# Performance work log

Hardware: AMD Instinct MI355X
Metric: run time of the kernel (lower is better)

The kernel has to match this reference:

```python
import jax, jax.numpy as jnp
import numpy as np

BIG = 1e30  # finite stand-in for +inf to keep grads clean


def _chamfer_loss(bin_center, ground_truth):
    # bin_center: [B, n_bins, 1] 1-D 'point cloud' of bin centers
    # ground_truth: [B, 1, H, W] depth map
    B = bin_center.shape[0]
    c = bin_center[..., 0]                      # [B, nb]
    p = ground_truth.reshape(B, -1)             # [B, V] flattened depth points
    mask = p >= 0.001                           # valid (non-near-zero) depths
    n = jnp.sum(mask, axis=1)                   # [B] valid count per sample
    Lmax = jnp.max(n)                           # pad_sequence pads every sample to L_max
    npad = (Lmax - n).astype(c.dtype)           # number of zero pad-points per sample

    # pairwise squared distances between bin centers and depth points
    D = (c[:, :, None] - p[:, None, :]) ** 2    # [B, nb, V]

    # direction 1: gt points -> nearest bin center (sum over points)
    dmin_p = jnp.min(D, axis=1)                 # [B, V]
    sumA = jnp.sum(jnp.where(mask, dmin_p, 0.0), axis=1)
    # each zero pad-point contributes min_j c_j^2
    c2 = c ** 2                                 # [B, nb]
    sumA = sumA + npad * jnp.min(c2, axis=1)

    # direction 2: bin centers -> nearest gt point (incl. zero pad-points if any)
    Dm = jnp.where(mask[:, None, :], D, jnp.asarray(BIG, D.dtype))
    min_valid = jnp.min(Dm, axis=2)             # [B, nb] min over valid points
    has_pad = (npad > 0)[:, None]
    min_b = jnp.where(has_pad, jnp.minimum(min_valid, c2), min_valid)
    sumB = jnp.sum(min_b, axis=1)               # [B]

    # chamferdist: point_reduction=sum, batch_reduction=mean, bidirectional
    return jnp.mean(sumA + sumB)


def setup_inputs() -> dict:
    key = jax.random.key(0)
    k1, k2 = jax.random.split(key)
    bin_center = jax.random.uniform(k1, (4, 256, 1), dtype=jnp.float32)
    ground_truth = jax.random.uniform(k2, (4, 1, 352, 448), dtype=jnp.float32)
    return {"bin_center": bin_center, "ground_truth": ground_truth}


def reference(bin_center, ground_truth):
    return _chamfer_loss(bin_center, ground_truth)
```

## Files before the change

kernel.cpp:

```cpp
#include <hip/hip_runtime.h>

#define NB   256
#define TPB  256
#define NI   (NB + 1)
#define G    128
#define MINF 1e30f
#define CAPD 1e15f

__global__ __launch_bounds__(NB) void k_sort(const float* __restrict__ bc,
                                             float* __restrict__ sbins,
                                             unsigned* __restrict__ gmin,
                                             unsigned* __restrict__ gmax) {
    __shared__ float s[NB];
    const int tid = threadIdx.x, b = blockIdx.x;
    s[tid] = bc[b * NB + tid];
    for (int t = tid; t < NI; t += NB) {
        gmin[b * NI + t] = 0xFFFFFFFFu;
        gmax[b * NI + t] = 0u;
    }
    __syncthreads();
    for (int k = 2; k <= NB; k <<= 1)
        for (int j = k >> 1; j > 0; j >>= 1) {
            const int ixj = tid ^ j;
            if (ixj > tid) {
                const float a = s[tid], bv = s[ixj];
                if ((a > bv) == ((tid & k) == 0)) { s[tid] = bv; s[ixj] = a; }
            }
            __syncthreads();
        }
    sbins[b * NB + tid] = s[tid];
}

__global__ __launch_bounds__(TPB) void k_main(
    const float* __restrict__ sbins, const float* __restrict__ gt,
    int V, int CH,
    float* __restrict__ sumA_part, int* __restrict__ cnt_part,
    unsigned* __restrict__ gmin, unsigned* __restrict__ gmax)
{
    const int b   = blockIdx.x / G;
    const int blk = blockIdx.x % G;
    const int tid = threadIdx.x;
    const int start = blk * CH;
    const int cn = min(CH, V - start);
    const float* __restrict__ gp = gt + (size_t)b * V + start;

    __shared__ float    c[NB];
    __shared__ unsigned imn[NI], imx[NI];
    c[tid] = sbins[b * NB + tid];
    for (int t = tid; t < NI; t += TPB) { imn[t] = 0xFFFFFFFFu; imx[t] = 0u; }
    __syncthreads();

    float sum = 0.f; int cnt = 0;
    for (int i = tid; i < cn; i += TPB) {
        const float q = gp[i];
        if (q >= 0.001f) {
            int idx = 0;
            #pragma unroll
            for (int st = 128; st >= 1; st >>= 1)
                idx += (c[idx + st - 1] <= q) ? st : 0;
            idx += (c[idx] <= q) ? 1 : 0;
            const float dlo = (idx > 0)  ? (q - c[idx - 1]) : MINF;
            const float dhi = (idx < NB) ? (c[idx] - q)     : MINF;
            const float d = fminf(dlo, dhi);
            sum += d * d; ++cnt;
            atomicMin(&imn[idx], __float_as_uint(q));
            atomicMax(&imx[idx], __float_as_uint(q));
        }
    }
    __syncthreads();

    for (int t = tid; t < NI; t += TPB) {
        const unsigned lo = imn[t], hi = imx[t];
        if (lo != 0xFFFFFFFFu) atomicMin(&gmin[b * NI + t], lo);
        if (hi != 0u)          atomicMax(&gmax[b * NI + t], hi);
    }

    for (int off = 32; off; off >>= 1) {
        sum += __shfl_down(sum, off);
        cnt += __shfl_down(cnt, off);
    }
    __shared__ float r4[4]; __shared__ int i4[4];
    if ((tid & 63) == 0) { r4[tid >> 6] = sum; i4[tid >> 6] = cnt; }
    __syncthreads();
    if (tid == 0) {
        sumA_part[blockIdx.x] = r4[0] + r4[1] + r4[2] + r4[3];
        cnt_part [blockIdx.x] = i4[0] + i4[1] + i4[2] + i4[3];
    }
}

__global__ __launch_bounds__(TPB) void k_final(
    const float* __restrict__ sbins,
    const float* __restrict__ sumA_part, const int* __restrict__ cnt_part,
    const unsigned* __restrict__ gmin, const unsigned* __restrict__ gmax,
    int B, float* __restrict__ out)
{
    const int tid = threadIdx.x;
    __shared__ float pm[NB], sm[NB];
    __shared__ float r4[4]; __shared__ int i4[4]; __shared__ float q4[4];
    __shared__ float ssa[8]; __shared__ int sn[8];

    for (int bb = 0; bb < B; ++bb) {
        float s = 0.f; int cc = 0;
        for (int k = tid; k < G; k += TPB) {
            s  += sumA_part[bb * G + k];
            cc += cnt_part [bb * G + k];
        }
        for (int off = 32; off; off >>= 1) { s += __shfl_down(s, off); cc += __shfl_down(cc, off); }
        if ((tid & 63) == 0) { r4[tid >> 6] = s; i4[tid >> 6] = cc; }
        __syncthreads();
        if (tid == 0) { ssa[bb] = r4[0]+r4[1]+r4[2]+r4[3]; sn[bb] = i4[0]+i4[1]+i4[2]+i4[3]; }
        __syncthreads();
    }
    int Lmax = 0;
    for (int bb = 0; bb < B; ++bb) Lmax = max(Lmax, sn[bb]);

    float total = 0.f;
    for (int bb = 0; bb < B; ++bb) {
        const unsigned hib = gmax[bb * NI + tid];
        const unsigned lob = gmin[bb * NI + tid + 1];
        pm[tid] = (hib == 0u)          ? -MINF : __uint_as_float(hib);
        sm[tid] = (lob == 0xFFFFFFFFu) ?  MINF : __uint_as_float(lob);
        __syncthreads();
        for (int off = 1; off < NB; off <<= 1) {
            const float vp = pm[tid], vs = sm[tid];
            const float op = (tid >= off)     ? pm[tid - off] : -MINF;
            const float os = (tid + off < NB) ? sm[tid + off] :  MINF;
            __syncthreads();
            pm[tid] = fmaxf(vp, op);
            sm[tid] = fminf(vs, os);
            __syncthreads();
        }
        const float cj = sbins[bb * NB + tid];
        const float c2 = cj * cj;
        const float d  = fminf(fminf(cj - pm[tid], sm[tid] - cj), CAPD);
        float bm = d * d;
        const int npad = Lmax - sn[bb];
        if (npad > 0) bm = fminf(bm, c2);
        float s = bm, mc = c2;
        for (int off = 32; off; off >>= 1) {
            s  += __shfl_down(s, off);
            mc  = fminf(mc, __shfl_down(mc, off));
        }
        if ((tid & 63) == 0) { r4[tid >> 6] = s; q4[tid >> 6] = mc; }
        __syncthreads();
        if (tid == 0)
            total += ssa[bb]
                   + (float)npad * fminf(fminf(q4[0], q4[1]), fminf(q4[2], q4[3]))
                   + (r4[0] + r4[1] + r4[2] + r4[3]);
        __syncthreads();
    }
    if (tid == 0) out[0] = total / (float)B;
}

extern "C" void kernel_launch(void* const* d_in, const int* in_sizes, int n_in,
                              void* d_out, int out_size, void* d_ws, size_t ws_size,
                              hipStream_t stream) {
    const float* bc = (const float*)d_in[0];
    const float* gt = (const float*)d_in[1];
    const int B  = in_sizes[0] / NB;
    const int V  = in_sizes[1] / B;
    const int CH = (V + G - 1) / G;

    float*    sbins     = (float*)d_ws;
    float*    sumA_part = sbins + (size_t)B * NB;
    int*      cnt_part  = (int*)(sumA_part + (size_t)B * G);
    unsigned* gmin      = (unsigned*)(cnt_part + (size_t)B * G);
    unsigned* gmax      = gmin + (size_t)B * NI;

    k_sort <<<B, NB, 0, stream>>>(bc, sbins, gmin, gmax);
    k_main <<<B * G, TPB, 0, stream>>>(sbins, gt, V, CH,
                                       sumA_part, cnt_part, gmin, gmax);
    k_final<<<1, TPB, 0, stream>>>(sbins, sumA_part, cnt_part,
                                   gmin, gmax, B, (float*)d_out);
}
```

Measured before the change: 78.26 us.

## Fuse sort, main pass and final reduction into one kernel with last-block finish

Replaces the three kernels (bin sort, main pass, single-block final) with one fused kernel. Every block re-sorts the bins in shared memory and computes its own bin-to-point nearest distance from its local min/max tables, merging the result into a global per-bin atomicMin. The last block to finish, found with an atomic counter, performs the final reduction. This removes two kernel launches and the separate scan in the final kernel, at the cost of a redundant bitonic sort and prefix scan in every block plus an extra memset launch.

```diff
diff --git a/kernel.cpp b/kernel.cpp
--- a/kernel.cpp
+++ b/kernel.cpp
@@ -7,49 +7,46 @@
 #define MINF 1e30f
 #define CAPD 1e15f
 
-__global__ __launch_bounds__(NB) void k_sort(const float* __restrict__ bc,
-                                             float* __restrict__ sbins,
-                                             unsigned* __restrict__ gmin,
-                                             unsigned* __restrict__ gmax) {
-    __shared__ float s[NB];
-    const int tid = threadIdx.x, b = blockIdx.x;
-    s[tid] = bc[b * NB + tid];
-    for (int t = tid; t < NI; t += NB) {
-        gmin[b * NI + t] = 0xFFFFFFFFu;
-        gmax[b * NI + t] = 0u;
-    }
+__global__ __launch_bounds__(TPB) void k_fused(
+    const float* __restrict__ bc, const float* __restrict__ gt,
+    int B, int V, int CH,
+    unsigned* __restrict__ gbin,
+    unsigned* __restrict__ counter,
+    unsigned* __restrict__ ssort,
+    unsigned* __restrict__ sumP,
+    unsigned* __restrict__ cntP,
+    float* __restrict__ out)
+{
+    const int b   = blockIdx.x / G;
+    const int blk = blockIdx.x % G;
+    const int tid = threadIdx.x;
+
+    __shared__ float    c[NB];
+    __shared__ unsigned imn[NI], imx[NI];
+    __shared__ float    pm[NB], sm[NB];
+    __shared__ float r4[4]; __shared__ int i4[4]; __shared__ float q4[4];
+    __shared__ float ssa[8]; __shared__ int sn[8];
+    __shared__ unsigned s_old;
+
+    c[tid] = bc[b * NB + tid];
+    for (int t = tid; t < NI; t += TPB) { imn[t] = 0xFFFFFFFFu; imx[t] = 0u; }
     __syncthreads();
+
     for (int k = 2; k <= NB; k <<= 1)
         for (int j = k >> 1; j > 0; j >>= 1) {
             const int ixj = tid ^ j;
             if (ixj > tid) {
-                const float a = s[tid], bv = s[ixj];
-                if ((a > bv) == ((tid & k) == 0)) { s[tid] = bv; s[ixj] = a; }
+                const float a = c[tid], bv = c[ixj];
+                if ((a > bv) == ((tid & k) == 0)) { c[tid] = bv; c[ixj] = a; }
             }
             __syncthreads();
         }
-    sbins[b * NB + tid] = s[tid];
-}
 
-__global__ __launch_bounds__(TPB) void k_main(
-    const float* __restrict__ sbins, const float* __restrict__ gt,
-    int V, int CH,
-    float* __restrict__ sumA_part, int* __restrict__ cnt_part,
-    unsigned* __restrict__ gmin, unsigned* __restrict__ gmax)
-{
-    const int b   = blockIdx.x / G;
-    const int blk = blockIdx.x % G;
-    const int tid = threadIdx.x;
+    if (blk == 0) atomicExch(&ssort[b * NB + tid], __float_as_uint(c[tid]));
+
     const int start = blk * CH;
     const int cn = min(CH, V - start);
     const float* __restrict__ gp = gt + (size_t)b * V + start;
-
-    __shared__ float    c[NB];
-    __shared__ unsigned imn[NI], imx[NI];
-    c[tid] = sbins[b * NB + tid];
-    for (int t = tid; t < NI; t += TPB) { imn[t] = 0xFFFFFFFFu; imx[t] = 0u; }
-    __syncthreads();
-
     float sum = 0.f; int cnt = 0;
     for (int i = tid; i < cn; i += TPB) {
         const float q = gp[i];
@@ -69,41 +66,46 @@
     }
     __syncthreads();
 
-    for (int t = tid; t < NI; t += TPB) {
-        const unsigned lo = imn[t], hi = imx[t];
-        if (lo != 0xFFFFFFFFu) atomicMin(&gmin[b * NI + t], lo);
-        if (hi != 0u)          atomicMax(&gmax[b * NI + t], hi);
+    pm[tid] = (imx[tid]     == 0u)          ? -MINF : __uint_as_float(imx[tid]);
+    sm[tid] = (imn[tid + 1] == 0xFFFFFFFFu) ?  MINF : __uint_as_float(imn[tid + 1]);
+    __syncthreads();
+    for (int off = 1; off < NB; off <<= 1) {
+        const float vp = pm[tid], vs = sm[tid];
+        const float op = (tid >= off)     ? pm[tid - off] : -MINF;
+        const float os = (tid + off < NB) ? sm[tid + off] :  MINF;
+        __syncthreads();
+        pm[tid] = fmaxf(vp, op);
+        sm[tid] = fminf(vs, os);
+        __syncthreads();
+    }
+    {
+        const float cj = c[tid];
+        const float d  = fminf(fminf(cj - pm[tid], sm[tid] - cj), CAPD);
+        atomicMin(&gbin[b * NB + tid], __float_as_uint(d * d));
     }
 
     for (int off = 32; off; off >>= 1) {
         sum += __shfl_down(sum, off);
         cnt += __shfl_down(cnt, off);
     }
-    __shared__ float r4[4]; __shared__ int i4[4];
     if ((tid & 63) == 0) { r4[tid >> 6] = sum; i4[tid >> 6] = cnt; }
     __syncthreads();
     if (tid == 0) {
-        sumA_part[blockIdx.x] = r4[0] + r4[1] + r4[2] + r4[3];
-        cnt_part [blockIdx.x] = i4[0] + i4[1] + i4[2] + i4[3];
+        atomicExch(&sumP[blockIdx.x], __float_as_uint(r4[0] + r4[1] + r4[2] + r4[3]));
+        atomicExch(&cntP[blockIdx.x], (unsigned)(i4[0] + i4[1] + i4[2] + i4[3]));
     }
-}
 
-__global__ __launch_bounds__(TPB) void k_final(
-    const float* __restrict__ sbins,
-    const float* __restrict__ sumA_part, const int* __restrict__ cnt_part,
-    const unsigned* __restrict__ gmin, const unsigned* __restrict__ gmax,
-    int B, float* __restrict__ out)
-{
-    const int tid = threadIdx.x;
-    __shared__ float pm[NB], sm[NB];
-    __shared__ float r4[4]; __shared__ int i4[4]; __shared__ float q4[4];
-    __shared__ float ssa[8]; __shared__ int sn[8];
+    __syncthreads();
+    if (tid == 0) s_old = atomicAdd(counter, 1u);
+    __syncthreads();
+    if (s_old != (unsigned)(gridDim.x - 2)) return;
+    __threadfence();
 
     for (int bb = 0; bb < B; ++bb) {
         float s = 0.f; int cc = 0;
         for (int k = tid; k < G; k += TPB) {
-            s  += sumA_part[bb * G + k];
-            cc += cnt_part [bb * G + k];
+            s  += __uint_as_float(sumP[bb * G + k]);
+            cc += (int)cntP[bb * G + k];
         }
         for (int off = 32; off; off >>= 1) { s += __shfl_down(s, off); cc += __shfl_down(cc, off); }
         if ((tid & 63) == 0) { r4[tid >> 6] = s; i4[tid >> 6] = cc; }
@@ -116,25 +118,10 @@
 
     float total = 0.f;
     for (int bb = 0; bb < B; ++bb) {
-        const unsigned hib = gmax[bb * NI + tid];
-        const unsigned lob = gmin[bb * NI + tid + 1];
-        pm[tid] = (hib == 0u)          ? -MINF : __uint_as_float(hib);
-        sm[tid] = (lob == 0xFFFFFFFFu) ?  MINF : __uint_as_float(lob);
-        __syncthreads();
-        for (int off = 1; off < NB; off <<= 1) {
-            const float vp = pm[tid], vs = sm[tid];
-            const float op = (tid >= off)     ? pm[tid - off] : -MINF;
-            const float os = (tid + off < NB) ? sm[tid + off] :  MINF;
-            __syncthreads();
-            pm[tid] = fmaxf(vp, op);
-            sm[tid] = fminf(vs, os);
-            __syncthreads();
-        }
-        const float cj = sbins[bb * NB + tid];
+        const int   npad = Lmax - sn[bb];
+        const float cj = __uint_as_float(ssort[bb * NB + tid]);
         const float c2 = cj * cj;
-        const float d  = fminf(fminf(cj - pm[tid], sm[tid] - cj), CAPD);
-        float bm = d * d;
-        const int npad = Lmax - sn[bb];
+        float bm = __uint_as_float(gbin[bb * NB + tid]);
         if (npad > 0) bm = fminf(bm, c2);
         float s = bm, mc = c2;
         for (int off = 32; off; off >>= 1) {
@@ -161,15 +148,15 @@
     const int V  = in_sizes[1] / B;
     const int CH = (V + G - 1) / G;
 
-    float*    sbins     = (float*)d_ws;
-    float*    sumA_part = sbins + (size_t)B * NB;
-    int*      cnt_part  = (int*)(sumA_part + (size_t)B * G);
-    unsigned* gmin      = (unsigned*)(cnt_part + (size_t)B * G);
-    unsigned* gmax      = gmin + (size_t)B * NI;
+    unsigned* gbin    = (unsigned*)d_ws;
+    unsigned* counter = gbin + (size_t)B * NB;
+    unsigned* ssort   = counter + 1;
+    unsigned* sumP    = ssort + (size_t)B * NB;
+    unsigned* cntP    = sumP + (size_t)B * G;
 
-    k_sort <<<B, NB, 0, stream>>>(bc, sbins, gmin, gmax);
-    k_main <<<B * G, TPB, 0, stream>>>(sbins, gt, V, CH,
-                                       sumA_part, cnt_part, gmin, gmax);
-    k_final<<<1, TPB, 0, stream>>>(sbins, sumA_part, cnt_part,
-                                   gmin, gmax, B, (float*)d_out);
+    hipMemsetAsync(gbin, 0xFF, ((size_t)B * NB + 1) * sizeof(unsigned), stream);
+
+    k_fused<<<B * G, TPB, 0, stream>>>(bc, gt, B, V, CH,
+                                       gbin, counter, ssort, sumP, cntP,
+                                       (float*)d_out);
 }
```

Measured after the change: 79.45 us. About the same (+1.5%).
